# Performance work log

Hardware: AMD Instinct MI355X
Metric: run time of the kernel (lower is better)

The kernel has to match this reference:

```python
import jax, jax.numpy as jnp
import numpy as np

TAPS = 5
DELAY = 3
EPS_POWER = 1e-7   # clamp for inverse power (wpe_one_iteration eps)
EPS_REG = 1e-10    # diagonal loading of the correlation matrix


def setup_inputs() -> dict:
    key = jax.random.key(0)
    ks = jax.random.split(key, 5)
    B, F, C, T = 8, 257, 8, 800
    shp = (B, F, C, T)
    return {
        "data_sep_real": jax.random.normal(ks[0], shp, jnp.float32),
        "data_sep_imag": jax.random.normal(ks[1], shp, jnp.float32),
        "data_mix_real": jax.random.normal(ks[2], shp, jnp.float32),
        "data_mix_imag": jax.random.normal(ks[3], shp, jnp.float32),
        "ilens": jax.random.randint(ks[4], (B,), 1, T + 1, jnp.int32),
    }


def _ytilde(Y, taps, delay):
    # Y: (B,F,C,T) complex -> stacked delayed taps (B,F,taps*C,T)
    # tap k at time t holds Y[..., t - delay - k] (zero-padded past)
    B, F, C, T = Y.shape
    Yp = jnp.pad(Y, ((0, 0), (0, 0), (0, 0), (delay + taps - 1, 0)))
    tilde = jnp.stack(
        [Yp[..., taps - 1 - k: taps - 1 - k + T] for k in range(taps)], axis=2
    )  # (B,F,taps,C,T)
    return tilde.reshape(B, F, taps * C, T)


def _wpe_one_iteration(Y, power, taps, delay):
    # Y: (B,F,C,T) complex, power: (B,F,T) real
    B, F, C, T = Y.shape
    inv_power = 1.0 / jnp.maximum(power, EPS_POWER)          # (B,F,T)
    Yt = _ytilde(Y, taps, delay)                              # (B,F,K,T), K=taps*C
    t0 = delay + taps - 1                                     # correlations use t >= t0
    Ytv = Yt[..., t0:]
    Yv = Y[..., t0:]
    Ytw = Ytv * inv_power[:, :, None, t0:].astype(Y.dtype)
    # R = sum_t w(t) Ytilde(t) Ytilde(t)^H  -> (B,F,K,K)
    R = jnp.einsum('bfat,bfct->bfac', Ytw, jnp.conj(Ytv))
    # P = sum_t w(t) Ytilde(t) Y(t)^H      -> (B,F,K,C)
    P = jnp.einsum('bfat,bfet->bfae', Ytw, jnp.conj(Yv))
    K = taps * C
    R = R + EPS_REG * jnp.eye(K, dtype=R.dtype)
    G = jnp.linalg.solve(R, P)                                # (B,F,K,C)
    # X(t) = Y(t) - G^H Ytilde(t)
    X = Y - jnp.einsum('bfae,bfat->bfet', jnp.conj(G), Yt)
    return X


def reference(data_sep_real, data_sep_imag, data_mix_real, data_mix_imag, ilens):
    # power of separated signal, averaged over channels (use_dnn_mask=False)
    power = jnp.mean(data_sep_real ** 2 + data_sep_imag ** 2, axis=-2)  # (B,F,T)
    Ym = jax.lax.complex(data_mix_real, data_mix_imag)                  # (B,F,C,T)
    X = _wpe_one_iteration(Ym, power, TAPS, DELAY)
    # zero out padded frames: t >= ilens[b]
    t = jnp.arange(X.shape[-1])
    valid = t[None, :] < ilens[:, None]                                 # (B,T)
    X = jnp.where(valid[:, None, None, :], X, 0)
    # return real/imag stacked on last axis: (B,F,C,T,2)
    return jnp.stack([X.real, X.imag], axis=-1)
```

## Files before the change

kernel.cpp:

```cpp
#include <hip/hip_runtime.h>

#define B 8
#define F 257
#define C 8
#define T 800
#define TAPS 5
#define DELAY 3
#define K 40
#define NCOL 48
#define T0 7
#define BF (B*F)

typedef __bf16 bf16x8 __attribute__((ext_vector_type(8)));
typedef __bf16 bf16x4 __attribute__((ext_vector_type(4)));
typedef float f32x4 __attribute__((ext_vector_type(4)));

struct PF { float4 v[3]; };

__device__ __forceinline__ void dma16(const void* g, void* l) {
    __builtin_amdgcn_global_load_lds(
        (const __attribute__((address_space(1))) void*)g,
        (__attribute__((address_space(3))) void*)l, 16, 0, 0);
}

__global__ __launch_bounds__(256) void power_kernel(const float* __restrict__ sr,
                                                    const float* __restrict__ si,
                                                    float* __restrict__ W) {
    int bf = blockIdx.x;
    const float* srp = sr + (size_t)bf * C * T;
    const float* sip = si + (size_t)bf * C * T;
    int t0 = threadIdx.x * 4;
    if (t0 < T) {
        float s[4] = {0.f, 0.f, 0.f, 0.f};
#pragma unroll
        for (int c = 0; c < C; ++c) {
            float4 a = *(const float4*)(srp + c * T + t0);
            float4 b = *(const float4*)(sip + c * T + t0);
            s[0] = fmaf(a.x, a.x, fmaf(b.x, b.x, s[0]));
            s[1] = fmaf(a.y, a.y, fmaf(b.y, b.y, s[1]));
            s[2] = fmaf(a.z, a.z, fmaf(b.z, b.z, s[2]));
            s[3] = fmaf(a.w, a.w, fmaf(b.w, b.w, s[3]));
        }
        float4 w;
        float* wp = (float*)&w;
#pragma unroll
        for (int e = 0; e < 4; ++e) {
            float v = fmaxf(s[e] * (1.0f / C), 1e-7f);
            wp[e] = (t0 + e < T0) ? 0.f : rsqrtf(v);
        }
        *(float4*)(W + (size_t)bf * T + t0) = w;
    }
}

#define WB2 13824

__global__ __launch_bounds__(256, 2) void rp_mfma_kernel(const float* __restrict__ mr,
                                                         const float* __restrict__ mi,
                                                         const float* __restrict__ W,
                                                         float2* __restrict__ Rout,
                                                         float2* __restrict__ Pout) {
    __shared__ __align__(16) unsigned char SH[4 * WB2];
    const int lane = threadIdx.x & 63;
    const int wid = threadIdx.x >> 6;
    const int bf = blockIdx.x * 4 + wid;
    unsigned char* base = SH + wid * WB2;
    unsigned char* b0 = base + 7680;
    unsigned char* b1 = base + 10752;

    const float* mrp = mr + (size_t)bf * C * T;
    const float* mip = mi + (size_t)bf * C * T;
    const float* Wp  = W  + (size_t)bf * T;

    const int q = lane >> 4, col = lane & 15;
    const int pc = lane >> 3, pg = lane & 7;

    const int PM[6] = {0, 0, 0, 1, 1, 2};
    const int PN[6] = {0, 1, 2, 1, 2, 2};

    const float* sb[3];
    const float* sb0[3];
    bool hal[3];
#pragma unroll
    for (int it = 0; it < 3; ++it) {
        int task = lane + it * 64;
        hal[it] = false;
        if (task < 160) {
            int row = task / 10, grp = task - row * 10;
            int pl = row >> 3, c = row & 7;
            const float* cb = (pl ? mip : mrp) + c * T;
            sb[it] = cb + grp * 4 - 8;
            hal[it] = (grp < 2);
            sb0[it] = hal[it] ? cb : sb[it];
        } else if (task < 168) {
            sb[it] = Wp + (task - 160) * 4;
            sb0[it] = sb[it];
        } else {
            sb[it] = mrp + (task - 168) * 4;
            sb0[it] = sb[it];
        }
    }

    f32x4 accRe[6], accIr[6], accRi[6];
#pragma unroll
    for (int p = 0; p < 6; ++p) {
        accRe[p] = (f32x4){0.f, 0.f, 0.f, 0.f};
        accIr[p] = (f32x4){0.f, 0.f, 0.f, 0.f};
        accRi[p] = (f32x4){0.f, 0.f, 0.f, 0.f};
    }

#pragma unroll
    for (int it = 0; it < 3; ++it)
        dma16(sb0[it], b0 + (lane + it * 64) * 16);
    asm volatile("s_waitcnt vmcnt(0)" ::: "memory");
#pragma unroll
    for (int it = 0; it < 3; ++it) {
        int task = lane + it * 64;
        if (hal[it])
            *(float4*)(b0 + task * 16) = make_float4(0.f, 0.f, 0.f, 0.f);
    }
    __builtin_amdgcn_sched_barrier(0);

    for (int ks = 0; ks < 25; ++ks) {
        unsigned char* buf = (ks & 1) ? b1 : b0;
        unsigned char* nbuf = (ks & 1) ? b0 : b1;
        int ntb = (ks < 24) ? (ks + 1) * 32 : ks * 32;
#pragma unroll
        for (int it = 0; it < 3; ++it)
            dma16(sb[it] + ntb, nbuf + (lane + it * 64) * 16);
        asm volatile("s_waitcnt vmcnt(3)" ::: "memory");
        __builtin_amdgcn_sched_barrier(0);

        {
            const float* yrr = (const float*)(buf + pc * 160);
            const float* yir = (const float*)(buf + (8 + pc) * 160);
            float yre[12], yim[12];
            float4 r0 = *(const float4*)(yrr + pg * 4);
            float4 r1 = *(const float4*)(yrr + pg * 4 + 4);
            float4 r2 = *(const float4*)(yrr + pg * 4 + 8);
            float4 i0 = *(const float4*)(yir + pg * 4);
            float4 i1 = *(const float4*)(yir + pg * 4 + 4);
            float4 i2 = *(const float4*)(yir + pg * 4 + 8);
            yre[0] = r0.x; yre[1] = r0.y; yre[2]  = r0.z; yre[3]  = r0.w;
            yre[4] = r1.x; yre[5] = r1.y; yre[6]  = r1.z; yre[7]  = r1.w;
            yre[8] = r2.x; yre[9] = r2.y; yre[10] = r2.z; yre[11] = r2.w;
            yim[0] = i0.x; yim[1] = i0.y; yim[2]  = i0.z; yim[3]  = i0.w;
            yim[4] = i1.x; yim[5] = i1.y; yim[6]  = i1.z; yim[7]  = i1.w;
            yim[8] = i2.x; yim[9] = i2.y; yim[10] = i2.z; yim[11] = i2.w;
            float4 w4 = *(const float4*)(buf + 2560 + pg * 16);
            float wv[4] = {w4.x, w4.y, w4.z, w4.w};
#pragma unroll
            for (int v = 0; v < 6; ++v) {
                int row = (v < 5) ? (v * 8 + pc) : (40 + pc);
                int off = (v < 5) ? (5 - v) : 8;
                bf16x4 zr, zi;
#pragma unroll
                for (int e = 0; e < 4; ++e) {
                    zr[e] = (__bf16)(wv[e] * yre[off + e]);
                    zi[e] = (__bf16)(wv[e] * yim[off + e]);
                }
                *(bf16x4*)(base + row * 80 + pg * 8) = zr;
                *(bf16x4*)(base + 3840 + row * 80 + pg * 8) = zi;
            }
        }

        bf16x8 fr[3], fi[3];
#pragma unroll
        for (int X = 0; X < 3; ++X) {
            fr[X] = *(const bf16x8*)(base + (X * 16 + col) * 80 + q * 16);
            fi[X] = *(const bf16x8*)(base + 3840 + (X * 16 + col) * 80 + q * 16);
        }
#pragma unroll
        for (int p = 0; p < 6; ++p) {
            int mt = PM[p], nt = PN[p];
            accRe[p] = __builtin_amdgcn_mfma_f32_16x16x32_bf16(fr[mt], fr[nt], accRe[p], 0, 0, 0);
            accRe[p] = __builtin_amdgcn_mfma_f32_16x16x32_bf16(fi[mt], fi[nt], accRe[p], 0, 0, 0);
            accIr[p] = __builtin_amdgcn_mfma_f32_16x16x32_bf16(fi[mt], fr[nt], accIr[p], 0, 0, 0);
            accRi[p] = __builtin_amdgcn_mfma_f32_16x16x32_bf16(fr[mt], fi[nt], accRi[p], 0, 0, 0);
        }
    }

    float2* Rp = Rout + (size_t)bf * K * K;
    float2* Pp = Pout + (size_t)bf * K * C;
#pragma unroll
    for (int p = 0; p < 6; ++p) {
        int mt = PM[p], nt = PN[p];
#pragma unroll
        for (int r = 0; r < 4; ++r) {
            int m = mt * 16 + q * 4 + r;
            int n = nt * 16 + col;
            float re = accRe[p][r];
            float im = accIr[p][r] - accRi[p][r];
            if (m < K) {
                if (n < K) {
                    if (m == n) re += 1e-10f;
                    Rp[m * K + n] = make_float2(re, im);
                } else {
                    Pp[m * C + (n - K)] = make_float2(re, im);
                }
            }
            if (mt != nt && m < K && n < K)
                Rp[n * K + m] = make_float2(re, -im);
        }
    }
}

__device__ __forceinline__ float rdlane(float v, int j) {
    return __uint_as_float(__builtin_amdgcn_readlane(__float_as_uint(v), (unsigned)j));
}

__global__ __launch_bounds__(256) void solve_kernel(const float2* __restrict__ Rin,
                                                    const float2* __restrict__ Pin,
                                                    float2* __restrict__ Gout) {
    __shared__ float2 lbuf[2][64];
    const int bf = blockIdx.x;
    const int lane = threadIdx.x & 63;
    const int w = threadIdx.x >> 6;
    const bool act = lane < K;
    const int lr = act ? lane : 0;

    float2 colw[12];
    {
        const float2* Arow = Rin + (size_t)bf * K * K + (size_t)lr * K;
        const float2* Prow = Pin + (size_t)bf * K * C + (size_t)lr * C;
#pragma unroll
        for (int m = 0; m < 10; ++m) {
            float2 v = Arow[4 * m + w];
            colw[m] = act ? v : make_float2(0.f, 0.f);
        }
#pragma unroll
        for (int m = 10; m < 12; ++m) {
            float2 v = Prow[4 * (m - 10) + w];
            colw[m] = act ? v : make_float2(0.f, 0.f);
        }
    }

#pragma unroll
    for (int j = 0; j < K; ++j) {
        const int par = j & 1;
        const int wo = j & 3;
        const int mj = j >> 2;
        if (w == wo) {
            float dx = rdlane(colw[mj].x, j);
            float dy = rdlane(colw[mj].y, j);
            float den = fmaf(dx, dx, dy * dy);
            float r = 1.0f / den;
            float ix = dx * r, iy = -dy * r;
            float lx = colw[mj].x * ix - colw[mj].y * iy;
            float ly = colw[mj].x * iy + colw[mj].y * ix;
            bool isj = (lane == j);
            lx = isj ? (1.0f - ix) : lx;
            ly = isj ? (0.0f - iy) : ly;
            lbuf[par][lane] = make_float2(lx, ly);
        }
        __syncthreads();
        float2 l = lbuf[par][lane];
#pragma unroll
        for (int m = 0; m < 12; ++m) {
            if (4 * m + 3 <= j) continue;
            bool doit = (4 * m > j) || (4 * m + w > j);
            if (doit) {
                float ux = rdlane(colw[m].x, j);
                float uy = rdlane(colw[m].y, j);
                colw[m].x = fmaf(-l.x, ux, fmaf( l.y, uy, colw[m].x));
                colw[m].y = fmaf(-l.x, uy, fmaf(-l.y, ux, colw[m].y));
            }
        }
    }

    if (act) {
        float2* Gp = Gout + (size_t)bf * K * C + (size_t)lane * C;
        Gp[w]     = colw[10];
        Gp[4 + w] = colw[11];
    }
}

#define XSTR 144
#define XWB 12032

__device__ __forceinline__ PF x_load(const float* __restrict__ mrp,
                                     const float* __restrict__ mip,
                                     int tb, int lane) {
    PF p;
#pragma unroll
    for (int it = 0; it < 3; ++it) {
        int task = lane + it * 64;
        float4 v = make_float4(0.f, 0.f, 0.f, 0.f);
        if (task < 160) {
            int pl = task / 80;
            int rem = task - pl * 80;
            int c = rem / 10, grp = rem - c * 10;
            int tg = tb - 8 + grp * 4;
            const float* srcp = pl ? mip : mrp;
            if (tg >= 0) v = *(const float4*)(srcp + c * T + tg);
        }
        p.v[it] = v;
    }
    return p;
}

__device__ __forceinline__ void x_store(const PF& p, float* sre, float* sim_, int lane) {
#pragma unroll
    for (int it = 0; it < 3; ++it) {
        int task = lane + it * 64;
        if (task < 160) {
            int pl = task / 80;
            int rem = task - pl * 80;
            int c = rem / 10, grp = rem - c * 10;
            *(float4*)((pl ? sim_ : sre) + c * 44 + grp * 4) = p.v[it];
        }
    }
}

__global__ __launch_bounds__(64) void x_mfma_kernel(const float* __restrict__ mr,
                                                    const float* __restrict__ mi,
                                                    const float2* __restrict__ Gin,
                                                    const int* __restrict__ ilens,
                                                    float2* __restrict__ out) {
    __shared__ __align__(16) unsigned char SH[XWB];
    const int lane = threadIdx.x;
    const int gid = blockIdx.x;
    const int bf = gid >> 2;
    const int split = gid & 3;
    const int ck0 = (split == 0) ? 0 : (1 + split * 6);
    const int nck = (split == 0) ? 7 : 6;
    unsigned char* base = SH;
    float* sre = (float*)(base + 9216);
    float* sim_ = (float*)(base + 10624);

    const float* mrp = mr + (size_t)bf * C * T;
    const float* mip = mi + (size_t)bf * C * T;
    const float2* Gp = Gin + (size_t)bf * K * C;
    float2* outp = out + (size_t)bf * C * T;
    const int len = ilens[bf / F];

    const int q = lane >> 4, col = lane & 15;
    const int t2 = lane >> 1, half = lane & 1;

#pragma unroll
    for (int pl = 0; pl < 2; ++pl) {
        unsigned char* pb = base + pl * 4608 + t2 * XSTR + 80 + half * 24;
        *(float2*)(pb)      = make_float2(0.f, 0.f);
        *(float2*)(pb + 8)  = make_float2(0.f, 0.f);
        *(float2*)(pb + 16) = make_float2(0.f, 0.f);
    }

    bf16x8 Agr[2], Agi[2], Agin[2];
#pragma unroll
    for (int ks = 0; ks < 2; ++ks)
#pragma unroll
        for (int j = 0; j < 8; ++j) {
            int a = ks * 32 + q * 8 + j;
            float2 g = make_float2(0.f, 0.f);
            if (a < K && col < C) g = Gp[a * C + col];
            Agr[ks][j]  = (__bf16)g.x;
            Agi[ks][j]  = (__bf16)g.y;
            Agin[ks][j] = (__bf16)(-g.y);
        }

    PF cur = x_load(mrp, mip, ck0 * 32, lane);

    for (int ci = 0; ci < nck; ++ci) {
        const int tb = (ck0 + ci) * 32;

        x_store(cur, sre, sim_, lane);
        if (ci + 1 < nck) cur = x_load(mrp, mip, tb + 32, lane);

#pragma unroll
        for (int i = 0; i < 5; ++i) {
            int abase = half * 20 + 4 * i;
            bf16x4 zr, zi;
#pragma unroll
            for (int e2 = 0; e2 < 4; ++e2) {
                int a = abase + e2;
                int v = a >> 3, c = a & 7;
                int idx = c * 44 + t2 + 5 - v;
                zr[e2] = (__bf16)sre[idx];
                zi[e2] = (__bf16)sim_[idx];
            }
            *(bf16x4*)(base + t2 * XSTR + abase * 2) = zr;
            *(bf16x4*)(base + 4608 + t2 * XSTR + abase * 2) = zi;
        }

#pragma unroll
        for (int tt = 0; tt < 2; ++tt) {
            const int trow = tt * 16 + col;
            f32x4 accRe = (f32x4){0.f, 0.f, 0.f, 0.f};
            f32x4 accIm = (f32x4){0.f, 0.f, 0.f, 0.f};
#pragma unroll
            for (int ks = 0; ks < 2; ++ks) {
                bf16x8 byr = *(const bf16x8*)(base + trow * XSTR + ks * 64 + q * 16);
                bf16x8 byi = *(const bf16x8*)(base + 4608 + trow * XSTR + ks * 64 + q * 16);
                accRe = __builtin_amdgcn_mfma_f32_16x16x32_bf16(Agr[ks], byr, accRe, 0, 0, 0);
                accRe = __builtin_amdgcn_mfma_f32_16x16x32_bf16(Agi[ks], byi, accRe, 0, 0, 0);
                accIm = __builtin_amdgcn_mfma_f32_16x16x32_bf16(Agr[ks], byi, accIm, 0, 0, 0);
                accIm = __builtin_amdgcn_mfma_f32_16x16x32_bf16(Agin[ks], byr, accIm, 0, 0, 0);
            }
            if (q < 2) {
                int t = tb + tt * 16 + col;
                int l = tt * 16 + col + 8;
                bool ok = (t < len);
#pragma unroll
                for (int r = 0; r < 4; ++r) {
                    int e = q * 4 + r;
                    float yr = sre[e * 44 + l];
                    float yi = sim_[e * 44 + l];
                    float2 v = ok ? make_float2(yr - accRe[r], yi - accIm[r])
                                  : make_float2(0.f, 0.f);
                    outp[e * T + t] = v;
                }
            }
        }
    }
}

extern "C" void kernel_launch(void* const* d_in, const int* in_sizes, int n_in,
                              void* d_out, int out_size, void* d_ws, size_t ws_size,
                              hipStream_t stream) {
    const float* sep_r = (const float*)d_in[0];
    const float* sep_i = (const float*)d_in[1];
    const float* mix_r = (const float*)d_in[2];
    const float* mix_i = (const float*)d_in[3];
    const int* ilens   = (const int*)d_in[4];

    float* ws = (float*)d_ws;
    float* W = ws;
    float2* Rws = (float2*)(ws + (size_t)BF * T);
    float2* Gws = Rws + (size_t)BF * K * K;

    power_kernel<<<BF, 256, 0, stream>>>(sep_r, sep_i, W);
    rp_mfma_kernel<<<BF / 4, 256, 0, stream>>>(mix_r, mix_i, W, Rws, Gws);
    solve_kernel<<<BF, 256, 0, stream>>>(Rws, Gws, Gws);
    x_mfma_kernel<<<BF * 4, 64, 0, stream>>>(mix_r, mix_i, Gws, ilens, (float2*)d_out);
}
```

Measured before the change: 182.0 us.

## Shrink per-wave LDS staging to fit three blocks per CU

```diff
diff --git a/kernel.cpp b/kernel.cpp
--- a/kernel.cpp
+++ b/kernel.cpp
@@ -52,9 +52,9 @@
     }
 }
 
-#define WB2 13824
-
-__global__ __launch_bounds__(256, 2) void rp_mfma_kernel(const float* __restrict__ mr,
+#define WB2 12800
+
+__global__ __launch_bounds__(256, 3) void rp_mfma_kernel(const float* __restrict__ mr,
                                                          const float* __restrict__ mi,
                                                          const float* __restrict__ W,
                                                          float2* __restrict__ Rout,
@@ -65,7 +65,7 @@
     const int bf = blockIdx.x * 4 + wid;
     unsigned char* base = SH + wid * WB2;
     unsigned char* b0 = base + 7680;
-    unsigned char* b1 = base + 10752;
+    unsigned char* b1 = base + 10240;
 
     const float* mrp = mr + (size_t)bf * C * T;
     const float* mip = mi + (size_t)bf * C * T;
@@ -77,28 +77,28 @@
     const int PM[6] = {0, 0, 0, 1, 1, 2};
     const int PN[6] = {0, 1, 2, 1, 2, 2};
 
-    const float* sb[3];
-    const float* sb0[3];
-    bool hal[3];
-#pragma unroll
-    for (int it = 0; it < 3; ++it) {
+    const float* sdma[2]; const float* sdma0[2]; bool haldma[2];
+#pragma unroll
+    for (int it = 0; it < 2; ++it) {
         int task = lane + it * 64;
-        hal[it] = false;
-        if (task < 160) {
-            int row = task / 10, grp = task - row * 10;
-            int pl = row >> 3, c = row & 7;
-            const float* cb = (pl ? mip : mrp) + c * T;
-            sb[it] = cb + grp * 4 - 8;
-            hal[it] = (grp < 2);
-            sb0[it] = hal[it] ? cb : sb[it];
-        } else if (task < 168) {
-            sb[it] = Wp + (task - 160) * 4;
-            sb0[it] = sb[it];
-        } else {
-            sb[it] = mrp + (task - 168) * 4;
-            sb0[it] = sb[it];
-        }
-    }
+        int row = task / 10, grp = task - row * 10;
+        int pl = row >> 3, c = row & 7;
+        const float* cb = (pl ? mip : mrp) + c * T;
+        sdma[it] = cb + grp * 4 - 8;
+        haldma[it] = (grp < 2);
+        sdma0[it] = haldma[it] ? cb : sdma[it];
+    }
+    const bool tact = lane < 32;
+    {
+    }
+    int ttask = 128 + (tact ? lane : 0);
+    int trow = ttask / 10, tgrp = ttask - trow * 10;
+    int tpl = trow >> 3, tc = trow & 7;
+    const float* tcb = (tpl ? mip : mrp) + tc * T;
+    const float* tsrc = tcb + tgrp * 4 - 8;
+    const bool thal = (tgrp < 2);
+    const float* tsrc0 = thal ? tcb : tsrc;
+    const float* wsrc = Wp + pg * 4;
 
     f32x4 accRe[6], accIr[6], accRi[6];
 #pragma unroll
@@ -108,26 +108,28 @@
         accRi[p] = (f32x4){0.f, 0.f, 0.f, 0.f};
     }
 
-#pragma unroll
-    for (int it = 0; it < 3; ++it)
-        dma16(sb0[it], b0 + (lane + it * 64) * 16);
+    dma16(sdma0[0], b0 + lane * 16);
+    dma16(sdma0[1], b0 + 1024 + lane * 16);
+    float4 ty = tact ? *(const float4*)tsrc0 : make_float4(0.f, 0.f, 0.f, 0.f);
+    float4 wcur = *(const float4*)wsrc;
     asm volatile("s_waitcnt vmcnt(0)" ::: "memory");
 #pragma unroll
-    for (int it = 0; it < 3; ++it) {
-        int task = lane + it * 64;
-        if (hal[it])
-            *(float4*)(b0 + task * 16) = make_float4(0.f, 0.f, 0.f, 0.f);
-    }
+    for (int it = 0; it < 2; ++it)
+        if (haldma[it])
+            *(float4*)(b0 + it * 1024 + lane * 16) = make_float4(0.f, 0.f, 0.f, 0.f);
+    if (thal) ty = make_float4(0.f, 0.f, 0.f, 0.f);
     __builtin_amdgcn_sched_barrier(0);
 
     for (int ks = 0; ks < 25; ++ks) {
         unsigned char* buf = (ks & 1) ? b1 : b0;
         unsigned char* nbuf = (ks & 1) ? b0 : b1;
-        int ntb = (ks < 24) ? (ks + 1) * 32 : ks * 32;
-#pragma unroll
-        for (int it = 0; it < 3; ++it)
-            dma16(sb[it] + ntb, nbuf + (lane + it * 64) * 16);
-        asm volatile("s_waitcnt vmcnt(3)" ::: "memory");
+        if (tact) *(float4*)(buf + 2048 + lane * 16) = ty;
+        if (ks < 24) {
+            int ntb = (ks + 1) * 32;
+            dma16(sdma[0] + ntb, nbuf + lane * 16);
+            dma16(sdma[1] + ntb, nbuf + 1024 + lane * 16);
+        }
+        asm volatile("s_waitcnt vmcnt(2)" ::: "memory");
         __builtin_amdgcn_sched_barrier(0);
 
         {
@@ -146,8 +148,7 @@
             yim[0] = i0.x; yim[1] = i0.y; yim[2]  = i0.z; yim[3]  = i0.w;
             yim[4] = i1.x; yim[5] = i1.y; yim[6]  = i1.z; yim[7]  = i1.w;
             yim[8] = i2.x; yim[9] = i2.y; yim[10] = i2.z; yim[11] = i2.w;
-            float4 w4 = *(const float4*)(buf + 2560 + pg * 16);
-            float wv[4] = {w4.x, w4.y, w4.z, w4.w};
+            float wv[4] = {wcur.x, wcur.y, wcur.z, wcur.w};
 #pragma unroll
             for (int v = 0; v < 6; ++v) {
                 int row = (v < 5) ? (v * 8 + pc) : (40 + pc);
@@ -176,6 +177,12 @@
             accRe[p] = __builtin_amdgcn_mfma_f32_16x16x32_bf16(fi[mt], fi[nt], accRe[p], 0, 0, 0);
             accIr[p] = __builtin_amdgcn_mfma_f32_16x16x32_bf16(fi[mt], fr[nt], accIr[p], 0, 0, 0);
             accRi[p] = __builtin_amdgcn_mfma_f32_16x16x32_bf16(fr[mt], fi[nt], accRi[p], 0, 0, 0);
+        }
+
+        if (ks < 24) {
+            int ntb = (ks + 1) * 32;
+            if (tact) ty = *(const float4*)(tsrc + ntb);
+            wcur = *(const float4*)(wsrc + ntb);
         }
     }
 
```

New measurement: 175.4 us. 1.04x faster.
